# Performance work log

Hardware: AMD Instinct MI355X
Metric: run time of the kernel (lower is better)

The kernel has to match this reference:

```python
import jax, jax.numpy as jnp
import numpy as np
from jax import lax

N, S, F_IN = 50000, 16, 64
HID, HEADS = 128, 4
C = HID // HEADS  # 32
E = 1600000
NEG_SLOPE = 0.2


def setup_inputs() -> dict:
    key = jax.random.key(0)
    ks = jax.random.split(key, 16)
    sc = lambda *sh: 1.0 / np.sqrt(sh[-1])
    inp = {}
    inp['node_features_sequence'] = jax.random.normal(ks[0], (N, S, F_IN), dtype=jnp.float32)
    inp['edge_index'] = jax.random.randint(ks[1], (2, E), 0, N, dtype=jnp.int64)
    # GRU params (single layer, order r,z,n as in torch)
    inp['gru_w_ih'] = jax.random.normal(ks[2], (3 * HID, F_IN), jnp.float32) * sc(F_IN)
    inp['gru_w_hh'] = jax.random.normal(ks[3], (3 * HID, HID), jnp.float32) * sc(HID)
    inp['gru_b_ih'] = jax.random.normal(ks[4], (3 * HID,), jnp.float32) * 0.01
    inp['gru_b_hh'] = jax.random.normal(ks[5], (3 * HID,), jnp.float32) * 0.01
    # GAT layer 1
    inp['gat1_w'] = jax.random.normal(ks[6], (HID, HID), jnp.float32) * sc(HID)
    inp['gat1_a_src'] = jax.random.normal(ks[7], (HEADS, C), jnp.float32) * sc(C)
    inp['gat1_a_dst'] = jax.random.normal(ks[8], (HEADS, C), jnp.float32) * sc(C)
    inp['gat1_b'] = jnp.zeros((HID,), jnp.float32)
    # GAT layer 2
    inp['gat2_w'] = jax.random.normal(ks[9], (HID, HID), jnp.float32) * sc(HID)
    inp['gat2_a_src'] = jax.random.normal(ks[10], (HEADS, C), jnp.float32) * sc(C)
    inp['gat2_a_dst'] = jax.random.normal(ks[11], (HEADS, C), jnp.float32) * sc(C)
    inp['gat2_b'] = jnp.zeros((HID,), jnp.float32)
    # classifier
    inp['clf_w'] = jax.random.normal(ks[12], (1, HID), jnp.float32) * sc(HID)
    inp['clf_b'] = jnp.zeros((1,), jnp.float32)
    return inp


def gru_last(xs, w_ih, w_hh, b_ih, b_hh):
    # xs: [N, S, F] -> last hidden [N, H]
    n, _, _ = xs.shape
    h_dim = w_hh.shape[1]
    gi_all = jnp.einsum('nsf,gf->nsg', xs, w_ih) + b_ih  # [N,S,3H]
    gi_all = jnp.swapaxes(gi_all, 0, 1)  # [S,N,3H]

    def step(h, gi):
        gh = h @ w_hh.T + b_hh
        i_r, i_z, i_n = jnp.split(gi, 3, axis=-1)
        h_r, h_z, h_n = jnp.split(gh, 3, axis=-1)
        r = jax.nn.sigmoid(i_r + h_r)
        z = jax.nn.sigmoid(i_z + h_z)
        nn_ = jnp.tanh(i_n + r * h_n)
        h_new = (1.0 - z) * nn_ + z * h
        return h_new, None

    h0 = jnp.zeros((n, h_dim), xs.dtype)
    h_last, _ = lax.scan(step, h0, gi_all)
    return h_last


def gat_layer(x, src, dst, w, a_src, a_dst, b):
    # x: [N, HID]; PyG GATConv with add_self_loops, concat heads
    n = x.shape[0]
    h = (x @ w.T).reshape(n, HEADS, C)  # [N,H,C]
    a_s = jnp.einsum('nhc,hc->nh', h, a_src)  # [N,H]
    a_d = jnp.einsum('nhc,hc->nh', h, a_dst)
    e = jax.nn.leaky_relu(a_s[src] + a_d[dst], NEG_SLOPE)  # [E',H]
    m = jax.ops.segment_max(e, dst, num_segments=n)
    m = jnp.where(jnp.isfinite(m), m, 0.0)
    ex = jnp.exp(e - m[dst])
    denom = jax.ops.segment_sum(ex, dst, num_segments=n)
    alpha = ex / (denom[dst] + 1e-16)  # [E',H]
    msg = h[src] * alpha[:, :, None]  # [E',H,C]
    out = jax.ops.segment_sum(msg, dst, num_segments=n)  # [N,H,C]
    return out.reshape(n, HEADS * C) + b


def reference(node_features_sequence, edge_index,
              gru_w_ih, gru_w_hh, gru_b_ih, gru_b_hh,
              gat1_w, gat1_a_src, gat1_a_dst, gat1_b,
              gat2_w, gat2_a_src, gat2_a_dst, gat2_b,
              clf_w, clf_b):
    n = node_features_sequence.shape[0]
    # add self loops once (same structure for both layers)
    loops = jnp.arange(n, dtype=edge_index.dtype)
    src = jnp.concatenate([edge_index[0], loops])
    dst = jnp.concatenate([edge_index[1], loops])

    x = gru_last(node_features_sequence, gru_w_ih, gru_w_hh, gru_b_ih, gru_b_hh)
    x = jax.nn.elu(gat_layer(x, src, dst, gat1_w, gat1_a_src, gat1_a_dst, gat1_b))
    x = jax.nn.elu(gat_layer(x, src, dst, gat2_w, gat2_a_src, gat2_a_dst, gat2_b))
    return jax.nn.sigmoid(x @ clf_w.T + clf_b)  # [N,1]
```

## Files before the change

### kernel.cpp

```cpp
#include <hip/hip_runtime.h>
#include <hip/hip_bf16.h>
#include <hip/hip_fp16.h>
#include <math.h>

#define N_NODES 50000
#define NP      50048
#define SEQ     16
#define FIN     64
#define HID     128
#define NEDGE   1600000
#define NB_SCAN 196
#define AGG_CAP 96

typedef __attribute__((ext_vector_type(8))) short short8;
typedef __attribute__((ext_vector_type(4))) float f32x4;

__device__ __forceinline__ float lrelu02(float v) { return v > 0.f ? v : 0.2f * v; }
__device__ __forceinline__ float frcp(float v) { return __builtin_amdgcn_rcpf(v); }
__device__ __forceinline__ float sigmoidf_(float v) { return frcp(1.f + __expf(-v)); }
__device__ __forceinline__ float eluf_(float v) { return v > 0.f ? v : (__expf(v) - 1.f); }

__device__ __forceinline__ unsigned bfpk(float lo, float hi) {
    union { __hip_bfloat162 h; unsigned u; } c;
    c.h = __float22bfloat162_rn(make_float2(lo, hi));
    return c.u;
}
__device__ __forceinline__ unsigned hfpk(float lo, float hi) {
    union { __half2 h; unsigned u; } c;
    c.h = __float22half2_rn(make_float2(lo, hi));
    return c.u;
}
__device__ __forceinline__ float2 h2f2(unsigned u) {
    union { unsigned u; __half2 h; } c;
    c.u = u;
    return __half22float2(c.h);
}
__device__ __forceinline__ short8 pack8(float4 a, float4 b) {
    union { short8 s; unsigned u[4]; } r;
    r.u[0] = bfpk(a.x, a.y); r.u[1] = bfpk(a.z, a.w);
    r.u[2] = bfpk(b.x, b.y); r.u[3] = bfpk(b.z, b.w);
    return r.s;
}

__global__ __launch_bounds__(512, 2) void gru_fused(
    const float* __restrict__ x,
    const float* __restrict__ w_ih,
    const float* __restrict__ w_hh,
    const float* __restrict__ b_ih,
    const float* __restrict__ b_hh,
    float* __restrict__ hout)
{
    __shared__ __align__(16) short hA[2][32][72];
    __shared__ __align__(16) short xB[2][32][72];

    const int tid  = threadIdx.x;
    const int wave = tid >> 6;
    const int lane = tid & 63;
    const int q    = lane >> 4;
    const int rl   = lane & 15;
    const int n0   = blockIdx.x * 32;
    const int ch   = wave * 16 + rl;

    short8 whhf[3][4];
    short8 wihf[3][2];
#pragma unroll
    for (int g = 0; g < 3; g++) {
        int row = g * 128 + ch;
#pragma unroll
        for (int kc = 0; kc < 4; kc++) {
            const float* p = w_hh + row * HID + kc * 32 + q * 8;
            whhf[g][kc] = pack8(*(const float4*)p, *(const float4*)(p + 4));
        }
#pragma unroll
        for (int kc = 0; kc < 2; kc++) {
            const float* p = w_ih + row * FIN + kc * 32 + q * 8;
            wihf[g][kc] = pack8(*(const float4*)p, *(const float4*)(p + 4));
        }
    }

    const float br  = b_ih[ch] + b_hh[ch];
    const float bz  = b_ih[128 + ch] + b_hh[128 + ch];
    const float bin = b_ih[256 + ch];
    const float bhn = b_hh[256 + ch];

    const int sn = tid >> 4;
    const int sk = (tid & 15) * 4;
    int sgn = n0 + sn; if (sgn > N_NODES - 1) sgn = N_NODES - 1;
    const float* xsp = x + (size_t)sgn * SEQ * FIN + sk;

    float hreg[2][4];
#pragma unroll
    for (int mt = 0; mt < 2; mt++)
#pragma unroll
        for (int r = 0; r < 4; r++) hreg[mt][r] = 0.f;

    {
        float4 v = *(const float4*)(xsp);
        int2 pv;
        pv.x = (int)bfpk(v.x, v.y);
        pv.y = (int)bfpk(v.z, v.w);
        *(int2*)&xB[0][sn][sk] = pv;
    }
    __syncthreads();

    for (int t = 0; t < SEQ; t++) {
        const int xb = t & 1;
        short8 xf[2][2], hf[2][4];
#pragma unroll
        for (int mt = 0; mt < 2; mt++)
#pragma unroll
            for (int kc = 0; kc < 2; kc++)
                xf[mt][kc] = *(const short8*)&xB[xb][mt * 16 + rl][kc * 32 + q * 8];
        if (t > 0) {
            const int hb = (t - 1) & 1;
#pragma unroll
            for (int mt = 0; mt < 2; mt++)
#pragma unroll
                for (int kc = 0; kc < 4; kc++)
                    hf[mt][kc] = *(const short8*)&hA[hb][mt * 16 + rl][kc * 32 + q * 8];
        }

        float4 xs;
        if (t + 1 < SEQ) xs = *(const float4*)(xsp + (t + 1) * FIN);

        f32x4 accr[2], accz[2], accin[2], acchn[2];
#pragma unroll
        for (int mt = 0; mt < 2; mt++) {
            accr[mt] = (f32x4)0.f; accz[mt] = (f32x4)0.f;
            accin[mt] = (f32x4)0.f; acchn[mt] = (f32x4)0.f;
#pragma unroll
            for (int kc = 0; kc < 2; kc++) {
                accr[mt]  = __builtin_amdgcn_mfma_f32_16x16x32_bf16(xf[mt][kc], wihf[0][kc], accr[mt], 0, 0, 0);
                accz[mt]  = __builtin_amdgcn_mfma_f32_16x16x32_bf16(xf[mt][kc], wihf[1][kc], accz[mt], 0, 0, 0);
                accin[mt] = __builtin_amdgcn_mfma_f32_16x16x32_bf16(xf[mt][kc], wihf[2][kc], accin[mt], 0, 0, 0);
            }
            if (t > 0) {
#pragma unroll
                for (int kc = 0; kc < 4; kc++) {
                    accr[mt]  = __builtin_amdgcn_mfma_f32_16x16x32_bf16(hf[mt][kc], whhf[0][kc], accr[mt], 0, 0, 0);
                    accz[mt]  = __builtin_amdgcn_mfma_f32_16x16x32_bf16(hf[mt][kc], whhf[1][kc], accz[mt], 0, 0, 0);
                    acchn[mt] = __builtin_amdgcn_mfma_f32_16x16x32_bf16(hf[mt][kc], whhf[2][kc], acchn[mt], 0, 0, 0);
                }
            }
        }

        if (t + 1 < SEQ) {
            int2 pv;
            pv.x = (int)bfpk(xs.x, xs.y);
            pv.y = (int)bfpk(xs.z, xs.w);
            *(int2*)&xB[(t + 1) & 1][sn][sk] = pv;
        }

        const int b = t & 1;
#pragma unroll
        for (int mt = 0; mt < 2; mt++) {
            float hv[4];
#pragma unroll
            for (int r = 0; r < 4; r++) {
                float rg = sigmoidf_(accr[mt][r] + br);
                float zg = sigmoidf_(accz[mt][r] + bz);
                float a  = accin[mt][r] + bin + rg * (acchn[mt][r] + bhn);
                float e  = __expf(2.f * a);
                float nn = 1.f - 2.f * frcp(e + 1.f);
                float h  = zg * (hreg[mt][r] - nn) + nn;
                hreg[mt][r] = h;
                hv[r] = h;
            }
            unsigned u01 = bfpk(hv[0], hv[1]);
            unsigned u23 = bfpk(hv[2], hv[3]);
            const int nb = mt * 16 + q * 4;
            hA[b][nb + 0][ch] = (short)(u01 & 0xFFFF);
            hA[b][nb + 1][ch] = (short)(u01 >> 16);
            hA[b][nb + 2][ch] = (short)(u23 & 0xFFFF);
            hA[b][nb + 3][ch] = (short)(u23 >> 16);
        }
        __syncthreads();
    }

#pragma unroll
    for (int mt = 0; mt < 2; mt++)
#pragma unroll
        for (int r = 0; r < 4; r++)
            hout[(size_t)(n0 + mt * 16 + q * 4 + r) * HID + ch] = hreg[mt][r];
}

__global__ void prep_weights(const float* __restrict__ g1w, const float* __restrict__ g2w,
                             float* __restrict__ g1T, float* __restrict__ g2T)
{
    int i = blockIdx.x * 256 + threadIdx.x;
    if (i < 128 * 128) {
        int k = i >> 7, g = i & 127;
        g1T[i] = g1w[g * 128 + k];
        g2T[i] = g2w[g * 128 + k];
    }
}

__global__ void count_edges(const int* __restrict__ dst, int* __restrict__ deg, int e)
{
    int i = blockIdx.x * 256 + threadIdx.x;
    if (i < e) atomicAdd(&deg[dst[i]], 1);
}

__device__ __forceinline__ int block_scan_inc(int v)
{
    int tid = threadIdx.x, lane = tid & 63, w = tid >> 6;
#pragma unroll
    for (int off = 1; off < 64; off <<= 1) {
        int tmp = __shfl_up(v, off, 64);
        if (lane >= off) v += tmp;
    }
    __shared__ int wsum[4];
    if (lane == 63) wsum[w] = v;
    __syncthreads();
    int add = 0;
    for (int i = 0; i < w; i++) add += wsum[i];
    return v + add;
}

__global__ void scan_block_sums(const int* __restrict__ deg, int* __restrict__ bsum, int n)
{
    int i = blockIdx.x * 256 + threadIdx.x;
    int v = (i < n) ? deg[i] : 0;
#pragma unroll
    for (int off = 32; off >= 1; off >>= 1) v += __shfl_xor(v, off, 64);
    __shared__ int ws[4];
    if ((threadIdx.x & 63) == 0) ws[threadIdx.x >> 6] = v;
    __syncthreads();
    if (threadIdx.x == 0) bsum[blockIdx.x] = ws[0] + ws[1] + ws[2] + ws[3];
}

__global__ void scan_bsum(int* __restrict__ bsum, int nb)
{
    int tid = threadIdx.x;
    int v = (tid < nb) ? bsum[tid] : 0;
    v = block_scan_inc(v);
    if (tid < nb) bsum[tid] = v;
}

__global__ void scan_final(const int* __restrict__ deg, const int* __restrict__ bsum,
                           int* __restrict__ rp, int n)
{
    int i = blockIdx.x * 256 + threadIdx.x;
    int v = (i < n) ? deg[i] : 0;
    int s = block_scan_inc(v);
    int add = (blockIdx.x > 0) ? bsum[blockIdx.x - 1] : 0;
    if (i < n) rp[i + 1] = s + add;
    if (i == 0) rp[0] = 0;
}

__global__ void fill_edges(const int* __restrict__ src, const int* __restrict__ dst,
                           const int* __restrict__ rp, int* __restrict__ cur,
                           int* __restrict__ col, int e)
{
    int i = blockIdx.x * 256 + threadIdx.x;
    if (i < e) {
        int d = dst[i];
        int pos = atomicAdd(&cur[d], 1);
        col[rp[d] + pos] = src[i];
    }
}

__global__ __launch_bounds__(256) void proj_attn(
    const float* __restrict__ x, const float* __restrict__ wT,
    const float* __restrict__ a_src, const float* __restrict__ a_dst,
    unsigned* __restrict__ hph, float* __restrict__ as_, float* __restrict__ ad_)
{
    __shared__ float xt[32][33];
    __shared__ float wt[32][128];
    __shared__ float ot[32][132];
    const int tid = threadIdx.x;
    const int tx = tid & 7;
    const int ty = tid >> 3;
    const int n0 = blockIdx.x * 32;
    float acc[4][4];
#pragma unroll
    for (int i = 0; i < 4; i++)
#pragma unroll
        for (int j = 0; j < 4; j++) acc[i][j] = 0.f;

    for (int k0 = 0; k0 < 128; k0 += 32) {
        __syncthreads();
#pragma unroll
        for (int i = 0; i < 4; i++) {
            int flat = tid + i * 256;
            int n = flat >> 5, k = flat & 31;
            xt[n][k] = x[(n0 + n) * HID + k0 + k];
        }
#pragma unroll
        for (int i = 0; i < 16; i++) {
            int flat = tid + i * 256;
            int kk = flat >> 7, g = flat & 127;
            wt[kk][g] = wT[(k0 + kk) * HID + g];
        }
        __syncthreads();
#pragma unroll 8
        for (int kk = 0; kk < 32; kk++) {
            float xv[4];
#pragma unroll
            for (int i = 0; i < 4; i++) xv[i] = xt[tx * 4 + i][kk];
            float4 wv = *(const float4*)&wt[kk][ty * 4];
#pragma unroll
            for (int i = 0; i < 4; i++) {
                acc[i][0] = fmaf(xv[i], wv.x, acc[i][0]);
                acc[i][1] = fmaf(xv[i], wv.y, acc[i][1]);
                acc[i][2] = fmaf(xv[i], wv.z, acc[i][2]);
                acc[i][3] = fmaf(xv[i], wv.w, acc[i][3]);
            }
        }
    }
#pragma unroll
    for (int i = 0; i < 4; i++) {
        int node = tx * 4 + i;
        ot[node][ty * 4 + 0] = acc[i][0];
        ot[node][ty * 4 + 1] = acc[i][1];
        ot[node][ty * 4 + 2] = acc[i][2];
        ot[node][ty * 4 + 3] = acc[i][3];
        uint2 pv;
        pv.x = hfpk(acc[i][0], acc[i][1]);
        pv.y = hfpk(acc[i][2], acc[i][3]);
        *(uint2*)&hph[(size_t)(n0 + node) * 64 + ty * 2] = pv;
    }
    __syncthreads();
    if (tid < 128) {
        int node = tid >> 2, head = tid & 3;
        const float* ar = a_src + head * 32;
        const float* br = a_dst + head * 32;
        float s = 0.f, d = 0.f;
#pragma unroll
        for (int j = 0; j < 32; j += 4) {
            float4 hv = *(const float4*)&ot[node][head * 32 + j];
            float4 av = *(const float4*)&ar[j];
            float4 bv = *(const float4*)&br[j];
            s += hv.x * av.x + hv.y * av.y + hv.z * av.z + hv.w * av.w;
            d += hv.x * bv.x + hv.y * bv.y + hv.z * bv.z + hv.w * bv.w;
        }
        as_[(n0 + node) * 4 + head] = s;
        ad_[(n0 + node) * 4 + head] = d;
    }
}

template <bool CLF>
__global__ __launch_bounds__(256) void gat_agg(
    const unsigned* __restrict__ hph, const float* __restrict__ as_,
    const float* __restrict__ ad_, const int* __restrict__ rp,
    const int* __restrict__ col, const float* __restrict__ bias,
    float* __restrict__ out, const float* __restrict__ cw,
    const float* __restrict__ cb, int n_nodes)
{
    __shared__ float exl[4][AGG_CAP][4];
    const int widx = threadIdx.x >> 6;
    const int lane = threadIdx.x & 63;
    const int n = blockIdx.x * 4 + widx;
    if (n >= n_nodes) return;

    const int e0 = rp[n], e1 = rp[n + 1];
    const int deg = e1 - e0;
    float4 adv = *(const float4*)&ad_[n * 4];
    float4 asn = *(const float4*)&as_[n * 4];
    float xs0 = __expf(lrelu02(asn.x + adv.x)), xs1 = __expf(lrelu02(asn.y + adv.y));
    float xs2 = __expf(lrelu02(asn.z + adv.z)), xs3 = __expf(lrelu02(asn.w + adv.w));

    float d0 = 0.f, d1 = 0.f, d2 = 0.f, d3 = 0.f;
    for (int e = e0 + lane; e < e1; e += 64) {
        int s = col[e];
        float4 a = *(const float4*)&as_[s * 4];
        float x0 = __expf(lrelu02(a.x + adv.x));
        float x1 = __expf(lrelu02(a.y + adv.y));
        float x2 = __expf(lrelu02(a.z + adv.z));
        float x3 = __expf(lrelu02(a.w + adv.w));
        int idx = e - e0;
        if (idx < AGG_CAP) {
            exl[widx][idx][0] = x0; exl[widx][idx][1] = x1;
            exl[widx][idx][2] = x2; exl[widx][idx][3] = x3;
        }
        d0 += x0; d1 += x1; d2 += x2; d3 += x3;
    }
#pragma unroll
    for (int off = 32; off >= 1; off >>= 1) {
        d0 += __shfl_xor(d0, off, 64);
        d1 += __shfl_xor(d1, off, 64);
        d2 += __shfl_xor(d2, off, 64);
        d3 += __shfl_xor(d3, off, 64);
    }
    d0 += xs0; d1 += xs1; d2 += xs2; d3 += xs3;
    float i0 = frcp(d0 + 1e-16f), i1 = frcp(d1 + 1e-16f);
    float i2 = frcp(d2 + 1e-16f), i3 = frcp(d3 + 1e-16f);

    const int head = lane >> 4;
    float invh = (head == 0) ? i0 : (head == 1) ? i1 : (head == 2) ? i2 : i3;
    float exsh = (head == 0) ? xs0 : (head == 1) ? xs1 : (head == 2) ? xs2 : xs3;
    float adh  = (head == 0) ? adv.x : (head == 1) ? adv.y : (head == 2) ? adv.z : adv.w;

    float2 sv = h2f2(hph[(size_t)n * 64 + lane]);
    float acc0 = exsh * sv.x;
    float acc1 = exsh * sv.y;

    if (deg <= AGG_CAP) {
        int e = e0;
        for (; e + 4 <= e1; e += 4) {
            int s_[4]; float w_[4]; unsigned u_[4];
#pragma unroll
            for (int u = 0; u < 4; u++) {
                s_[u] = col[e + u];
                w_[u] = exl[widx][e + u - e0][head];
            }
#pragma unroll
            for (int u = 0; u < 4; u++)
                u_[u] = hph[(size_t)s_[u] * 64 + lane];
#pragma unroll
            for (int u = 0; u < 4; u++) {
                float2 f = h2f2(u_[u]);
                acc0 = fmaf(w_[u], f.x, acc0);
                acc1 = fmaf(w_[u], f.y, acc1);
            }
        }
        for (; e < e1; e++) {
            int s = col[e];
            float w = exl[widx][e - e0][head];
            float2 f = h2f2(hph[(size_t)s * 64 + lane]);
            acc0 = fmaf(w, f.x, acc0);
            acc1 = fmaf(w, f.y, acc1);
        }
    } else {
        for (int e = e0; e < e1; e++) {
            int s = col[e];
            int idx = e - e0;
            float w;
            if (idx < AGG_CAP) w = exl[widx][idx][head];
            else               w = __expf(lrelu02(as_[s * 4 + head] + adh));
            float2 f = h2f2(hph[(size_t)s * 64 + lane]);
            acc0 = fmaf(w, f.x, acc0);
            acc1 = fmaf(w, f.y, acc1);
        }
    }

    float2 b2 = *(const float2*)&bias[2 * lane];
    float o0 = eluf_(acc0 * invh + b2.x);
    float o1 = eluf_(acc1 * invh + b2.y);
    if (CLF) {
        float2 cwv = *(const float2*)&cw[2 * lane];
        float v = o0 * cwv.x + o1 * cwv.y;
#pragma unroll
        for (int off = 32; off >= 1; off >>= 1) v += __shfl_xor(v, off, 64);
        if (lane == 0) out[n] = sigmoidf_(v + cb[0]);
    } else {
        *(float2*)&out[(size_t)n * HID + 2 * lane] = make_float2(o0, o1);
    }
}

extern "C" void kernel_launch(void* const* d_in, const int* in_sizes, int n_in,
                              void* d_out, int out_size, void* d_ws, size_t ws_size,
                              hipStream_t stream)
{
    const float* x     = (const float*)d_in[0];
    const int*   ei    = (const int*)d_in[1];
    const float* w_ih  = (const float*)d_in[2];
    const float* w_hh  = (const float*)d_in[3];
    const float* b_ih  = (const float*)d_in[4];
    const float* b_hh  = (const float*)d_in[5];
    const float* g1w   = (const float*)d_in[6];
    const float* g1as  = (const float*)d_in[7];
    const float* g1ad  = (const float*)d_in[8];
    const float* g1b   = (const float*)d_in[9];
    const float* g2w   = (const float*)d_in[10];
    const float* g2as  = (const float*)d_in[11];
    const float* g2ad  = (const float*)d_in[12];
    const float* g2b   = (const float*)d_in[13];
    const float* cw    = (const float*)d_in[14];
    const float* cb    = (const float*)d_in[15];
    float* out = (float*)d_out;

    char* wsb = (char*)d_ws;
    size_t off = 0;
    auto alc = [&](size_t bytes) { size_t o = off; off += (bytes + 255) & ~(size_t)255; return o; };

    float*    bufA = (float*)(wsb + alc((size_t)NP * HID * 4));
    float*    bufC = (float*)(wsb + alc((size_t)NP * HID * 4));
    unsigned* hph  = (unsigned*)(wsb + alc((size_t)NP * 64 * 4));
    float*    as_  = (float*)(wsb + alc((size_t)NP * 4 * 4));
    float*    ad_  = (float*)(wsb + alc((size_t)NP * 4 * 4));
    float*    g1T  = (float*)(wsb + alc((size_t)128 * 128 * 4));
    float*    g2T  = (float*)(wsb + alc((size_t)128 * 128 * 4));
    int*      rp   = (int*)(wsb + alc((size_t)(N_NODES + 1) * 4));
    int*      deg  = (int*)(wsb + alc((size_t)N_NODES * 4));
    int*      cur  = (int*)(wsb + alc((size_t)N_NODES * 4));
    int*      col  = (int*)(wsb + alc((size_t)NEDGE * 4));
    int*      bsum = (int*)(wsb + alc((size_t)256 * 4));

    const int* src = ei;
    const int* dst = ei + NEDGE;

    hipMemsetAsync(deg, 0, (size_t)N_NODES * 4, stream);
    hipMemsetAsync(cur, 0, (size_t)N_NODES * 4, stream);

    prep_weights<<<64, 256, 0, stream>>>(g1w, g2w, g1T, g2T);

    count_edges<<<NEDGE / 256, 256, 0, stream>>>(dst, deg, NEDGE);
    scan_block_sums<<<NB_SCAN, 256, 0, stream>>>(deg, bsum, N_NODES);
    scan_bsum<<<1, 256, 0, stream>>>(bsum, NB_SCAN);
    scan_final<<<NB_SCAN, 256, 0, stream>>>(deg, bsum, rp, N_NODES);
    fill_edges<<<NEDGE / 256, 256, 0, stream>>>(src, dst, rp, cur, col, NEDGE);

    gru_fused<<<NP / 32, 512, 0, stream>>>(x, w_ih, w_hh, b_ih, b_hh, bufA);

    proj_attn<<<NP / 32, 256, 0, stream>>>(bufA, g1T, g1as, g1ad, hph, as_, ad_);
    gat_agg<false><<<(N_NODES + 3) / 4, 256, 0, stream>>>(hph, as_, ad_, rp, col, g1b, bufC,
                                                          nullptr, nullptr, N_NODES);

    proj_attn<<<NP / 32, 256, 0, stream>>>(bufC, g2T, g2as, g2ad, hph, as_, ad_);
    gat_agg<true><<<(N_NODES + 3) / 4, 256, 0, stream>>>(hph, as_, ad_, rp, col, g2b, out,
                                                         cw, cb, N_NODES);
}
```

Before: 867.1 us.

## Interleave two independent GRU node groups per block to overlap phases

Each GRU block now handles 64 nodes as two independent 32-node groups and alternates timestep phases between them. The hidden-state LDS writes and next-x staging for one group are deferred into the other group's phase, so each barrier separates independent work. The aim is to hide LDS round-trip and barrier latency in the sequential recurrence behind the other group's MFMA and gate math. The cost is twice the shared memory, more live registers, and half as many blocks in the grid, which may worsen tail balance across CUs. The hidden-state LDS row width also grows from 72 to 136 shorts, matching the 128 channels written per row.

```diff
diff --git a/kernel.cpp b/kernel.cpp
--- a/kernel.cpp
+++ b/kernel.cpp
@@ -50,15 +50,15 @@
     const float* __restrict__ b_hh,
     float* __restrict__ hout)
 {
-    __shared__ __align__(16) short hA[2][32][72];
-    __shared__ __align__(16) short xB[2][32][72];
+    __shared__ __align__(16) short hA[2][2][32][136];
+    __shared__ __align__(16) short xB[2][2][32][72];
 
     const int tid  = threadIdx.x;
     const int wave = tid >> 6;
     const int lane = tid & 63;
     const int q    = lane >> 4;
     const int rl   = lane & 15;
-    const int n0   = blockIdx.x * 32;
+    const int n0   = blockIdx.x * 64;
     const int ch   = wave * 16 + rl;
 
     short8 whhf[3][4];
@@ -85,103 +85,121 @@
 
     const int sn = tid >> 4;
     const int sk = (tid & 15) * 4;
-    int sgn = n0 + sn; if (sgn > N_NODES - 1) sgn = N_NODES - 1;
-    const float* xsp = x + (size_t)sgn * SEQ * FIN + sk;
-
-    float hreg[2][4];
-#pragma unroll
-    for (int mt = 0; mt < 2; mt++)
-#pragma unroll
-        for (int r = 0; r < 4; r++) hreg[mt][r] = 0.f;
+    int g0n = n0 + sn;      if (g0n > N_NODES - 1) g0n = N_NODES - 1;
+    int g1n = n0 + 32 + sn; if (g1n > N_NODES - 1) g1n = N_NODES - 1;
+    const float* xs0 = x + (size_t)g0n * SEQ * FIN + sk;
+    const float* xs1 = x + (size_t)g1n * SEQ * FIN + sk;
+
+    float hreg[2][2][4];
+#pragma unroll
+    for (int g = 0; g < 2; g++)
+#pragma unroll
+        for (int mt = 0; mt < 2; mt++)
+#pragma unroll
+            for (int r = 0; r < 4; r++) hreg[g][mt][r] = 0.f;
+
+    unsigned hp01[2], hp23[2];
+    float4 xhold;
 
     {
-        float4 v = *(const float4*)(xsp);
+        float4 v = *(const float4*)(xs0);
         int2 pv;
         pv.x = (int)bfpk(v.x, v.y);
         pv.y = (int)bfpk(v.z, v.w);
-        *(int2*)&xB[0][sn][sk] = pv;
-    }
+        *(int2*)&xB[0][0][sn][sk] = pv;
+    }
+    xhold = *(const float4*)(xs1);
     __syncthreads();
 
+#define GRU_PHASE(G, DO_HW, HWB, DO_XW, XWB, DO_XL, XLP)                          \
+    {                                                                             \
+        const int rb = (t - 1) & 1;                                               \
+        short8 xf[2][2], hf[2][4];                                                \
+        _Pragma("unroll")                                                         \
+        for (int mt = 0; mt < 2; mt++)                                            \
+            _Pragma("unroll")                                                     \
+            for (int kc = 0; kc < 2; kc++)                                        \
+                xf[mt][kc] = *(const short8*)&xB[G][t & 1][mt * 16 + rl][kc * 32 + q * 8]; \
+        if (t > 0) {                                                              \
+            _Pragma("unroll")                                                     \
+            for (int mt = 0; mt < 2; mt++)                                        \
+                _Pragma("unroll")                                                 \
+                for (int kc = 0; kc < 4; kc++)                                    \
+                    hf[mt][kc] = *(const short8*)&hA[G][rb][mt * 16 + rl][kc * 32 + q * 8]; \
+        }                                                                         \
+                         \
+        if (DO_HW) {                                                              \
+            _Pragma("unroll")                                                     \
+            for (int mt = 0; mt < 2; mt++) {                                      \
+                const int nb = mt * 16 + q * 4;                                   \
+                hA[G ^ 1][HWB][nb + 0][ch] = (short)(hp01[mt] & 0xFFFF);          \
+                hA[G ^ 1][HWB][nb + 1][ch] = (short)(hp01[mt] >> 16);             \
+                hA[G ^ 1][HWB][nb + 2][ch] = (short)(hp23[mt] & 0xFFFF);          \
+                hA[G ^ 1][HWB][nb + 3][ch] = (short)(hp23[mt] >> 16);             \
+            }                                                                     \
+        }                                                                         \
+        if (DO_XW) {                                                              \
+            int2 pv;                                                              \
+            pv.x = (int)bfpk(xhold.x, xhold.y);                                   \
+            pv.y = (int)bfpk(xhold.z, xhold.w);                                   \
+            *(int2*)&xB[G ^ 1][XWB][sn][sk] = pv;                                 \
+        }                                                                         \
+        if (DO_XL) xhold = *(const float4*)(XLP);        \
+        f32x4 accr[2], accz[2], accin[2], acchn[2];                               \
+        _Pragma("unroll")                                                         \
+        for (int mt = 0; mt < 2; mt++) {                                          \
+            accr[mt] = (f32x4)0.f; accz[mt] = (f32x4)0.f;                         \
+            accin[mt] = (f32x4)0.f; acchn[mt] = (f32x4)0.f;                       \
+            _Pragma("unroll")                                                     \
+            for (int kc = 0; kc < 2; kc++) {                                      \
+                accr[mt]  = __builtin_amdgcn_mfma_f32_16x16x32_bf16(xf[mt][kc], wihf[0][kc], accr[mt], 0, 0, 0);  \
+                accz[mt]  = __builtin_amdgcn_mfma_f32_16x16x32_bf16(xf[mt][kc], wihf[1][kc], accz[mt], 0, 0, 0);  \
+                accin[mt] = __builtin_amdgcn_mfma_f32_16x16x32_bf16(xf[mt][kc], wihf[2][kc], accin[mt], 0, 0, 0); \
+            }                                                                     \
+            if (t > 0) {                                                          \
+                _Pragma("unroll")                                                 \
+                for (int kc = 0; kc < 4; kc++) {                                  \
+                    accr[mt]  = __builtin_amdgcn_mfma_f32_16x16x32_bf16(hf[mt][kc], whhf[0][kc], accr[mt], 0, 0, 0);  \
+                    accz[mt]  = __builtin_amdgcn_mfma_f32_16x16x32_bf16(hf[mt][kc], whhf[1][kc], accz[mt], 0, 0, 0);  \
+                    acchn[mt] = __builtin_amdgcn_mfma_f32_16x16x32_bf16(hf[mt][kc], whhf[2][kc], acchn[mt], 0, 0, 0); \
+                }                                                                 \
+            }                                                                     \
+        }                                                                         \
+        _Pragma("unroll")                                                         \
+        for (int mt = 0; mt < 2; mt++) {                                          \
+            float hv[4];                                                          \
+            _Pragma("unroll")                                                     \
+            for (int r = 0; r < 4; r++) {                                         \
+                float rg = sigmoidf_(accr[mt][r] + br);                           \
+                float zg = sigmoidf_(accz[mt][r] + bz);                           \
+                float a  = accin[mt][r] + bin + rg * (acchn[mt][r] + bhn);        \
+                float e  = __expf(2.f * a);                                       \
+                float nn = 1.f - 2.f * frcp(e + 1.f);                             \
+                float h  = zg * (hreg[G][mt][r] - nn) + nn;                       \
+                hreg[G][mt][r] = h;                                               \
+                hv[r] = h;                                                        \
+            }                                                                     \
+            hp01[mt] = bfpk(hv[0], hv[1]);                                        \
+            hp23[mt] = bfpk(hv[2], hv[3]);                                        \
+        }                                                                         \
+        __syncthreads();                                                          \
+    }
+
     for (int t = 0; t < SEQ; t++) {
-        const int xb = t & 1;
-        short8 xf[2][2], hf[2][4];
+        GRU_PHASE(0, (t > 0), ((t - 1) & 1), 1, (t & 1),
+                  (t + 1 < SEQ), (xs0 + (t + 1) * FIN))
+        GRU_PHASE(1, 1, (t & 1), (t + 1 < SEQ), ((t + 1) & 1),
+                  (t + 1 < SEQ), (xs1 + (t + 1) * FIN))
+    }
+#undef GRU_PHASE
+
+#pragma unroll
+    for (int g = 0; g < 2; g++)
 #pragma unroll
         for (int mt = 0; mt < 2; mt++)
 #pragma unroll
-            for (int kc = 0; kc < 2; kc++)
-                xf[mt][kc] = *(const short8*)&xB[xb][mt * 16 + rl][kc * 32 + q * 8];
-        if (t > 0) {
-            const int hb = (t - 1) & 1;
-#pragma unroll
-            for (int mt = 0; mt < 2; mt++)
-#pragma unroll
-                for (int kc = 0; kc < 4; kc++)
-                    hf[mt][kc] = *(const short8*)&hA[hb][mt * 16 + rl][kc * 32 + q * 8];
-        }
-
-        float4 xs;
-        if (t + 1 < SEQ) xs = *(const float4*)(xsp + (t + 1) * FIN);
-
-        f32x4 accr[2], accz[2], accin[2], acchn[2];
-#pragma unroll
-        for (int mt = 0; mt < 2; mt++) {
-            accr[mt] = (f32x4)0.f; accz[mt] = (f32x4)0.f;
-            accin[mt] = (f32x4)0.f; acchn[mt] = (f32x4)0.f;
-#pragma unroll
-            for (int kc = 0; kc < 2; kc++) {
-                accr[mt]  = __builtin_amdgcn_mfma_f32_16x16x32_bf16(xf[mt][kc], wihf[0][kc], accr[mt], 0, 0, 0);
-                accz[mt]  = __builtin_amdgcn_mfma_f32_16x16x32_bf16(xf[mt][kc], wihf[1][kc], accz[mt], 0, 0, 0);
-                accin[mt] = __builtin_amdgcn_mfma_f32_16x16x32_bf16(xf[mt][kc], wihf[2][kc], accin[mt], 0, 0, 0);
-            }
-            if (t > 0) {
-#pragma unroll
-                for (int kc = 0; kc < 4; kc++) {
-                    accr[mt]  = __builtin_amdgcn_mfma_f32_16x16x32_bf16(hf[mt][kc], whhf[0][kc], accr[mt], 0, 0, 0);
-                    accz[mt]  = __builtin_amdgcn_mfma_f32_16x16x32_bf16(hf[mt][kc], whhf[1][kc], accz[mt], 0, 0, 0);
-                    acchn[mt] = __builtin_amdgcn_mfma_f32_16x16x32_bf16(hf[mt][kc], whhf[2][kc], acchn[mt], 0, 0, 0);
-                }
-            }
-        }
-
-        if (t + 1 < SEQ) {
-            int2 pv;
-            pv.x = (int)bfpk(xs.x, xs.y);
-            pv.y = (int)bfpk(xs.z, xs.w);
-            *(int2*)&xB[(t + 1) & 1][sn][sk] = pv;
-        }
-
-        const int b = t & 1;
-#pragma unroll
-        for (int mt = 0; mt < 2; mt++) {
-            float hv[4];
-#pragma unroll
-            for (int r = 0; r < 4; r++) {
-                float rg = sigmoidf_(accr[mt][r] + br);
-                float zg = sigmoidf_(accz[mt][r] + bz);
-                float a  = accin[mt][r] + bin + rg * (acchn[mt][r] + bhn);
-                float e  = __expf(2.f * a);
-                float nn = 1.f - 2.f * frcp(e + 1.f);
-                float h  = zg * (hreg[mt][r] - nn) + nn;
-                hreg[mt][r] = h;
-                hv[r] = h;
-            }
-            unsigned u01 = bfpk(hv[0], hv[1]);
-            unsigned u23 = bfpk(hv[2], hv[3]);
-            const int nb = mt * 16 + q * 4;
-            hA[b][nb + 0][ch] = (short)(u01 & 0xFFFF);
-            hA[b][nb + 1][ch] = (short)(u01 >> 16);
-            hA[b][nb + 2][ch] = (short)(u23 & 0xFFFF);
-            hA[b][nb + 3][ch] = (short)(u23 >> 16);
-        }
-        __syncthreads();
-    }
-
-#pragma unroll
-    for (int mt = 0; mt < 2; mt++)
-#pragma unroll
-        for (int r = 0; r < 4; r++)
-            hout[(size_t)(n0 + mt * 16 + q * 4 + r) * HID + ch] = hreg[mt][r];
+            for (int r = 0; r < 4; r++)
+                hout[(size_t)(n0 + g * 32 + mt * 16 + q * 4 + r) * HID + ch] = hreg[g][mt][r];
 }
 
 __global__ void prep_weights(const float* __restrict__ g1w, const float* __restrict__ g2w,
@@ -501,7 +519,7 @@
     scan_final<<<NB_SCAN, 256, 0, stream>>>(deg, bsum, rp, N_NODES);
     fill_edges<<<NEDGE / 256, 256, 0, stream>>>(src, dst, rp, cur, col, NEDGE);
 
-    gru_fused<<<NP / 32, 512, 0, stream>>>(x, w_ih, w_hh, b_ih, b_hh, bufA);
+    gru_fused<<<NP / 64, 512, 0, stream>>>(x, w_ih, w_hh, b_ih, b_hh, bufA);
 
     proj_attn<<<NP / 32, 256, 0, stream>>>(bufA, g1T, g1as, g1ad, hph, as_, ad_);
     gat_agg<false><<<(N_NODES + 3) / 4, 256, 0, stream>>>(hph, as_, ad_, rp, col, g1b, bufC,
```

Measured after the change: 839.3 us. 3.2% less time.
